# Optimization experiments

Hardware: AMD Instinct MI355X
Metric: run time of the kernel (lower is better)

Reference implementation:

```python
import jax, jax.numpy as jnp
import numpy as np

PI = np.float32(np.pi)
CNOT = jnp.array([[1,0,0,0],[0,1,0,0],[0,0,0,1],[0,0,1,0]], dtype=jnp.complex64)


def _u3(t, p, l):
    c, s = jnp.cos(t / 2), jnp.sin(t / 2)
    return jnp.stack([
        jnp.stack([c + 0j, -jnp.exp(1j * l) * s]),
        jnp.stack([jnp.exp(1j * p) * s, jnp.exp(1j * (p + l)) * c]),
    ]).astype(jnp.complex64)


def _ry(t):
    c, s = jnp.cos(t / 2), jnp.sin(t / 2)
    return jnp.stack([jnp.stack([c, -s]), jnp.stack([s, c])]).astype(jnp.complex64)


def _rz(t):
    z = jnp.zeros((), jnp.complex64)
    return jnp.stack([
        jnp.stack([jnp.exp(-1j * t / 2).astype(jnp.complex64), z]),
        jnp.stack([z, jnp.exp(1j * t / 2).astype(jnp.complex64)]),
    ]).astype(jnp.complex64)


def _apply1(psi, G, w):
    # psi: [N,2,2,2,2]; uniform single-qubit gate G [2,2] on wire w
    psi = jnp.moveaxis(psi, 1 + w, -1)
    psi = jnp.einsum('ij,nabcj->nabci', G, psi)
    return jnp.moveaxis(psi, -1, 1 + w)


def _apply1_batch(psi, G, w):
    # per-sample gate G [N,2,2]
    psi = jnp.moveaxis(psi, 1 + w, -1)
    psi = jnp.einsum('nij,nabcj->nabci', G, psi)
    return jnp.moveaxis(psi, -1, 1 + w)


def _apply2(psi, G, a, b):
    # two-qubit gate G [4,4] on wires (a,b)
    psi = jnp.moveaxis(psi, (1 + a, 1 + b), (-2, -1))
    psi = psi.reshape(psi.shape[:-2] + (4,))
    psi = jnp.einsum('ij,nabj->nabi', G, psi)
    psi = psi.reshape(psi.shape[:-1] + (2, 2))
    return jnp.moveaxis(psi, (-2, -1), (1 + a, 1 + b))


def _su4(psi, u3s, angs, a, b):
    # u3s: [4,3] = (w0, w1, w5, w6); angs: [3] = (w2, w3, w4)
    psi = _apply1(psi, _u3(u3s[0, 0], u3s[0, 1], u3s[0, 2]), a)
    psi = _apply1(psi, _u3(u3s[1, 0], u3s[1, 1], u3s[1, 2]), b)
    psi = _apply2(psi, CNOT, a, b)
    psi = _apply1(psi, _ry(angs[0]), a)
    psi = _apply1(psi, _rz(angs[1]), b)
    psi = _apply2(psi, CNOT, b, a)
    psi = _apply1(psi, _ry(angs[2]), a)
    psi = _apply2(psi, CNOT, a, b)
    psi = _apply1(psi, _u3(u3s[2, 0], u3s[2, 1], u3s[2, 2]), a)
    psi = _apply1(psi, _u3(u3s[3, 0], u3s[3, 1], u3s[3, 2]), b)
    return psi


def _circuit(angles, qw_u3, qw_ang):
    # angles: [N,4]; returns PauliZ expvals [N,4]
    N = angles.shape[0]
    psi = jnp.zeros((N, 2, 2, 2, 2), jnp.complex64).at[:, 0, 0, 0, 0].set(1.0)
    for w in range(4):  # AngleEmbedding: RY(angle) on each wire, per-sample
        c, s = jnp.cos(angles[:, w] / 2), jnp.sin(angles[:, w] / 2)
        G = jnp.stack([jnp.stack([c, -s], -1), jnp.stack([s, c], -1)], -2).astype(jnp.complex64)
        psi = _apply1_batch(psi, G, w)
    pairs = [(0, 1), (1, 2), (2, 3), (3, 0)]
    for layer in range(2):
        u3s = qw_u3[4 * layer:4 * layer + 4]
        angs = qw_ang[3 * layer:3 * layer + 3]
        for (a, b) in pairs:
            psi = _su4(psi, u3s, angs, a, b)
    p = psi.real ** 2 + psi.imag ** 2  # [N,2,2,2,2]
    z = jnp.array([1.0, -1.0], p.dtype)
    evs = [jnp.sum(p * z.reshape([1] + [2 if i == w else 1 for i in range(4)]), axis=(1, 2, 3, 4)) for w in range(4)]
    return jnp.stack(evs, -1)


def _conv(x, w, b):
    y = jax.lax.conv_general_dilated(x, w, (1, 1), 'SAME', dimension_numbers=('NCHW', 'OIHW', 'NCHW'))
    return y + b[None, :, None, None]


def _maxpool2(x):
    return jax.lax.reduce_window(x, -jnp.inf, jax.lax.max, (1, 1, 2, 2), (1, 1, 2, 2), 'VALID')


def setup_inputs() -> dict:
    key = jax.random.key(0)
    ks = jax.random.split(key, 20)
    n = jax.random.normal
    return {
        'x': n(ks[0], (1024, 3, 32, 32), jnp.float32),
        'conv1_w': n(ks[1], (64, 3, 3, 3), jnp.float32) * 0.1,
        'conv1_b': n(ks[2], (64,), jnp.float32) * 0.1,
        'conv2_w': n(ks[3], (16, 64, 3, 3), jnp.float32) * 0.05,
        'conv2_b': n(ks[4], (16,), jnp.float32) * 0.1,
        'conv3_w': n(ks[5], (4, 16, 3, 3), jnp.float32) * 0.1,
        'conv3_b': n(ks[6], (4,), jnp.float32) * 0.1,
        'qw_u3': jax.random.uniform(ks[7], (8, 3), jnp.float32, 0.0, 2 * np.pi),
        'qw_ang': jax.random.uniform(ks[8], (6,), jnp.float32, 0.0, 2 * np.pi),
        'fc1a_w': n(ks[9], (64, 256), jnp.float32) * 0.06,
        'fc1a_b': n(ks[10], (64,), jnp.float32) * 0.1,
        'fc1b_w': n(ks[11], (128, 64), jnp.float32) * 0.1,
        'fc1b_b': n(ks[12], (128,), jnp.float32) * 0.1,
        'fc2a_w': n(ks[13], (64, 128), jnp.float32) * 0.1,
        'fc2a_b': n(ks[14], (64,), jnp.float32) * 0.1,
        'fc2b_w': n(ks[15], (10, 64), jnp.float32) * 0.1,
        'fc2b_b': n(ks[16], (10,), jnp.float32) * 0.1,
    }


def reference(x, conv1_w, conv1_b, conv2_w, conv2_b, conv3_w, conv3_b,
              qw_u3, qw_ang, fc1a_w, fc1a_b, fc1b_w, fc1b_b,
              fc2a_w, fc2a_b, fc2b_w, fc2b_b):
    h = _maxpool2(jax.nn.relu(_conv(x, conv1_w, conv1_b)))      # [B,64,16,16]
    h = _maxpool2(jax.nn.relu(_conv(h, conv2_w, conv2_b)))      # [B,16,8,8]
    h = jax.nn.leaky_relu(_conv(h, conv3_w, conv3_b), 0.01)     # [B,4,8,8]
    B, C, H, W = h.shape
    # 1x1 patches in (h, w, c) order, matching torch unfold+permute
    patches = jnp.transpose(h, (0, 2, 3, 1)).reshape(B * H * W, C)
    ang = jax.nn.sigmoid(patches) * PI
    q = _circuit(ang, qw_u3, qw_ang)            # [B*64, 4]
    q = q.reshape(B, H * W * 4)                 # [B, 256]
    h1 = jax.nn.relu(q @ fc1a_w.T + fc1a_b)
    h1 = h1 @ fc1b_w.T + fc1b_b
    h2 = jax.nn.relu(h1 @ fc2a_w.T + fc2a_b)
    return h2 @ fc2b_w.T + fc2b_b               # [B, 10]
```

## Files before the change

kernel.cpp:

```cpp
#include <hip/hip_runtime.h>
#include <math.h>

#define PI_F 3.14159265358979323846f

typedef _Float16 half2_t __attribute__((ext_vector_type(2)));
typedef _Float16 f16x8 __attribute__((ext_vector_type(8)));
typedef float f32x4v __attribute__((ext_vector_type(4)));

__device__ __forceinline__ unsigned packh2(float lo, float hi) {
  unsigned short l = __builtin_bit_cast(unsigned short, (_Float16)lo);
  unsigned short h = __builtin_bit_cast(unsigned short, (_Float16)hi);
  return (unsigned)l | ((unsigned)h << 16);
}

struct c2 { float x, y; };
__device__ __forceinline__ c2 cmul(c2 a, c2 b){ return c2{a.x*b.x - a.y*b.y, a.x*b.y + a.y*b.x}; }
__device__ __forceinline__ c2 cadd(c2 a, c2 b){ return c2{a.x+b.x, a.y+b.y}; }

__device__ __forceinline__ void rot2(c2 &a, c2 &b, c2 g00, c2 g01, c2 g10, c2 g11) {
  c2 na = cadd(cmul(g00,a), cmul(g01,b));
  c2 nb = cadd(cmul(g10,a), cmul(g11,b));
  a = na; b = nb;
}

__device__ __forceinline__ void mk_u3(float th, float ph, float la,
                                      c2 &g00, c2 &g01, c2 &g10, c2 &g11) {
  float ch = cosf(0.5f*th), sh = sinf(0.5f*th);
  float cl = cosf(la), sl = sinf(la);
  float cp = cosf(ph), sp = sinf(ph);
  float cpl = cp*cl - sp*sl, spl = sp*cl + cp*sl;
  g00 = c2{ch, 0.f};
  g01 = c2{-cl*sh, -sl*sh};
  g10 = c2{cp*sh, sp*sh};
  g11 = c2{cpl*ch, spl*ch};
}

template<int MA, int MB>
__device__ __forceinline__ void apply2q(c2 psi[16], const c2 M[16]) {
#pragma unroll
  for (int r = 0; r < 16; ++r) {
    if (r & (MA | MB)) continue;
    c2 a = psi[r], b = psi[r|MB], c = psi[r|MA], d = psi[r|MA|MB];
    psi[r]        = cadd(cadd(cmul(M[0],a),  cmul(M[1],b)),  cadd(cmul(M[2],c),  cmul(M[3],d)));
    psi[r|MB]     = cadd(cadd(cmul(M[4],a),  cmul(M[5],b)),  cadd(cmul(M[6],c),  cmul(M[7],d)));
    psi[r|MA]     = cadd(cadd(cmul(M[8],a),  cmul(M[9],b)),  cadd(cmul(M[10],c), cmul(M[11],d)));
    psi[r|MA|MB]  = cadd(cadd(cmul(M[12],a), cmul(M[13],b)), cadd(cmul(M[14],c), cmul(M[15],d)));
  }
}

__global__ __launch_bounds__(256) void k_setup(const float* __restrict__ w1a, const float* __restrict__ w1b,
                                               const float* __restrict__ w2a, const float* __restrict__ w2b,
                                               const float* __restrict__ c2w,
                                               const float* __restrict__ c1w, const float* __restrict__ c1b,
                                               const float* __restrict__ qw_u3,
                                               const float* __restrict__ qw_ang,
                                               float* __restrict__ wt, float* __restrict__ A) {
  __shared__ c2 SU[2][16];
  __shared__ float Ur[16*17], Ui[16*17];
  int t = threadIdx.x;
  if (blockIdx.x == 167) {
    if (t < 8) {
      int L = t >> 2, col = t & 3;
      c2 s[4];
#pragma unroll
      for (int i = 0; i < 4; ++i) s[i] = c2{(i==col)?1.f:0.f, 0.f};
      const float* u = qw_u3 + 12*L;
      const float* g = qw_ang + 3*L;
      c2 g00,g01,g10,g11;
      mk_u3(u[0],u[1],u[2], g00,g01,g10,g11);
      rot2(s[0],s[2], g00,g01,g10,g11); rot2(s[1],s[3], g00,g01,g10,g11);
      mk_u3(u[3],u[4],u[5], g00,g01,g10,g11);
      rot2(s[0],s[1], g00,g01,g10,g11); rot2(s[2],s[3], g00,g01,g10,g11);
      { c2 tmp = s[2]; s[2] = s[3]; s[3] = tmp; }
      { float c = cosf(0.5f*g[0]), sn = sinf(0.5f*g[0]);
        c2 r00{c,0.f}, r01{-sn,0.f}, r10{sn,0.f}, r11{c,0.f};
        rot2(s[0],s[2], r00,r01,r10,r11); rot2(s[1],s[3], r00,r01,r10,r11); }
      { float c = cosf(0.5f*g[1]), sn = sinf(0.5f*g[1]);
        c2 e0{c,-sn}, e1{c,sn};
        s[0]=cmul(s[0],e0); s[1]=cmul(s[1],e1); s[2]=cmul(s[2],e0); s[3]=cmul(s[3],e1); }
      { c2 tmp = s[1]; s[1] = s[3]; s[3] = tmp; }
      { float c = cosf(0.5f*g[2]), sn = sinf(0.5f*g[2]);
        c2 r00{c,0.f}, r01{-sn,0.f}, r10{sn,0.f}, r11{c,0.f};
        rot2(s[0],s[2], r00,r01,r10,r11); rot2(s[1],s[3], r00,r01,r10,r11); }
      { c2 tmp = s[2]; s[2] = s[3]; s[3] = tmp; }
      mk_u3(u[6],u[7],u[8], g00,g01,g10,g11);
      rot2(s[0],s[2], g00,g01,g10,g11); rot2(s[1],s[3], g00,g01,g10,g11);
      mk_u3(u[9],u[10],u[11], g00,g01,g10,g11);
      rot2(s[0],s[1], g00,g01,g10,g11); rot2(s[2],s[3], g00,g01,g10,g11);
#pragma unroll
      for (int k = 0; k < 4; ++k) SU[L][k*4 + col] = s[k];
    }
    __syncthreads();
    if (t < 16) {
      c2 psi[16];
#pragma unroll
      for (int i = 0; i < 16; ++i) psi[i] = c2{(i==t)?1.f:0.f, 0.f};
#pragma unroll
      for (int l = 0; l < 2; ++l) {
        c2 M[16];
#pragma unroll
        for (int k = 0; k < 16; ++k) M[k] = SU[l][k];
        apply2q<8,4>(psi, M);
        apply2q<4,2>(psi, M);
        apply2q<2,1>(psi, M);
        apply2q<1,8>(psi, M);
      }
#pragma unroll
      for (int k = 0; k < 16; ++k) { Ur[k*17+t] = psi[k].x; Ui[k*17+t] = psi[k].y; }
    }
    __syncthreads();
    {
      int i = t >> 4, j = t & 15;
      float a0=0.f,a1=0.f,a2=0.f,a3=0.f;
#pragma unroll
      for (int k = 0; k < 16; ++k) {
        float pr = Ur[k*17+i]*Ur[k*17+j] + Ui[k*17+i]*Ui[k*17+j];
        a0 += ((k>>3)&1) ? -pr : pr;
        a1 += ((k>>2)&1) ? -pr : pr;
        a2 += ((k>>1)&1) ? -pr : pr;
        a3 += ( k     &1) ? -pr : pr;
      }
      A[0*256 + t] = a0; A[1*256 + t] = a1; A[2*256 + t] = a2; A[3*256 + t] = a3;
    }
    return;
  }
  int id = blockIdx.x*256 + t;
  if (id < 16384) { int j = id >> 6, o = id & 63;  wt[id] = w1a[o*256 + j]; return; }
  int id1 = id - 16384;
  if (id1 < 8192)  { int j = id1 >> 7, o = id1 & 127; wt[16384 + id1] = w1b[o*64 + j]; return; }
  int id2 = id1 - 8192;
  if (id2 < 8192)  { int j = id2 >> 6, o = id2 & 63;  wt[24576 + id2] = w2a[o*128 + j]; return; }
  int id3 = id2 - 8192;
  if (id3 < 640)   { int j = id3 / 10, o = id3 % 10;  wt[32768 + id3] = w2b[o*64 + j]; return; }
  int id4 = id3 - 640;
  if (id4 < 4608) {
    int s = id4 >> 8, rem = id4 & 255, l = rem >> 2, r = rem & 3;
    int tap = s >> 1, h = s & 1;
    int oc = l & 15, j = l >> 4;
    int icl = 16*h + 4*j + r;
    float lo = c2w[oc*576 + icl*9 + tap];
    float hi = c2w[oc*576 + (icl+32)*9 + tap];
    ((unsigned*)wt)[33408 + id4] = packh2(lo, hi);
    return;
  }
  int id5 = id4 - 4608;
  if (id5 < 1024) {
    int nt = id5 >> 8, rem = id5 & 255, l = rem >> 2, r = rem & 3;
    int oc = nt*16 + (l & 15), j = l >> 4;
    int k0 = 8*j + 2*r;
    float lo = (k0     < 27) ? c1w[oc*27 + k0]     : 0.f;
    float hi = (k0 + 1 < 27) ? c1w[oc*27 + k0 + 1] : 0.f;
    ((unsigned*)wt)[38016 + id5] = packh2(lo, hi);
  }
}

__global__ __launch_bounds__(512, 2) void k_conv12(
    const float* __restrict__ x,
    const uint4* __restrict__ B1g, const float* __restrict__ b1,
    const uint4* __restrict__ B2g, const float* __restrict__ b2,
    float* __restrict__ h2) {
  __shared__ float xs[3480];
  __shared__ unsigned hsp[11664];
  int b = blockIdx.x, t = threadIdx.x;
  int l = t & 63, w = t >> 6;
  int m = l & 15, j = l >> 4;
  uint4 Bf1[4];
#pragma unroll
  for (int nt = 0; nt < 4; ++nt) Bf1[nt] = B1g[nt*64 + l];
  float bz1[4];
#pragma unroll
  for (int nt = 0; nt < 4; ++nt) bz1[nt] = b1[nt*16 + m];
  int offs[8]; bool valid[8];
#pragma unroll
  for (int q = 0; q < 8; ++q) {
    int kk = 8*j + q;
    valid[q] = (kk < 27);
    int kc = valid[q] ? kk : 0;
    int c = kc / 9, rem = kc - 9*c, wr = rem / 3, cc = rem - 3*wr;
    offs[q] = c*1156 + wr*34 + cc;
  }
  for (int i = t; i < 3480; i += 512) xs[i] = 0.f;
  {
    uint4 z = make_uint4(0u,0u,0u,0u);
    uint4* hz = (uint4*)hsp;
    for (int i = t; i < 2916; i += 512) hz[i] = z;
  }
  __syncthreads();
  for (int i = t; i < 3072; i += 512) {
    int c = i >> 10, rem = i & 1023, gy = rem >> 5, gx = rem & 31;
    xs[c*1156 + (gy+1)*34 + gx + 1] = x[(size_t)b*3072 + i];
  }
  __syncthreads();
#pragma unroll
  for (int h = 0; h < 2; ++h) {
    f32x4v acc[2][2][4];
#pragma unroll
    for (int rr = 0; rr < 2; ++rr)
#pragma unroll
      for (int xh = 0; xh < 2; ++xh)
#pragma unroll
        for (int nt = 0; nt < 4; ++nt)
          acc[rr][xh][nt] = f32x4v{bz1[nt], bz1[nt], bz1[nt], bz1[nt]};
#pragma unroll
    for (int rr = 0; rr < 2; ++rr)
#pragma unroll
      for (int xh = 0; xh < 2; ++xh) {
        int base = (16*h + 2*w + rr)*34 + 16*xh + m;
        float v[8];
#pragma unroll
        for (int q = 0; q < 8; ++q) v[q] = valid[q] ? xs[offs[q] + base] : 0.f;
        unsigned a0 = packh2(v[0], v[1]), a1 = packh2(v[2], v[3]);
        unsigned a2u = packh2(v[4], v[5]), a3 = packh2(v[6], v[7]);
        uint4 Au = make_uint4(a0, a1, a2u, a3);
        f16x8 Av = __builtin_bit_cast(f16x8, Au);
#pragma unroll
        for (int nt = 0; nt < 4; ++nt)
          acc[rr][xh][nt] = __builtin_amdgcn_mfma_f32_16x16x32_f16(
              Av, __builtin_bit_cast(f16x8, Bf1[nt]), acc[rr][xh][nt], 0, 0, 0);
      }
    {
      int pyg = 8*h + w;
#pragma unroll
      for (int ntp = 0; ntp < 2; ++ntp)
#pragma unroll
        for (int xh = 0; xh < 2; ++xh)
#pragma unroll
          for (int pv = 0; pv < 2; ++pv) {
            f32x4v aL0 = acc[0][xh][ntp],   aL1 = acc[1][xh][ntp];
            f32x4v aH0 = acc[0][xh][ntp+2], aH1 = acc[1][xh][ntp+2];
            float mlo = fmaxf(fmaxf(aL0[2*pv], aL0[2*pv+1]), fmaxf(aL1[2*pv], aL1[2*pv+1]));
            float mhi = fmaxf(fmaxf(aH0[2*pv], aH0[2*pv+1]), fmaxf(aH1[2*pv], aH1[2*pv+1]));
            int px = 8*xh + 2*j + pv;
            hsp[((pyg+1)*18 + px + 1)*36 + ntp*16 + m] =
                packh2(fmaxf(mlo, 0.f), fmaxf(mhi, 0.f));
          }
    }
  }
  __syncthreads();
  uint4 Bf2[18];
#pragma unroll
  for (int s = 0; s < 18; ++s) Bf2[s] = B2g[s*64 + l];
  float bz2 = b2[m];
  f32x4v a2[2];
  a2[0] = f32x4v{bz2, bz2, bz2, bz2};
  a2[1] = f32x4v{bz2, bz2, bz2, bz2};
#pragma unroll
  for (int s = 0; s < 18; ++s) {
    const int tap = s >> 1, hh = s & 1;
    const int dy = tap / 3, dx = tap % 3;
    f16x8 Bv = __builtin_bit_cast(f16x8, Bf2[s]);
#pragma unroll
    for (int tt = 0; tt < 2; ++tt) {
      int y = 2*w + tt;
      f16x8 Av = __builtin_bit_cast(f16x8,
          *(const uint4*)(hsp + ((y+dy)*18 + m + dx)*36 + 16*hh + 4*j));
      a2[tt] = __builtin_amdgcn_mfma_f32_16x16x32_f16(Av, Bv, a2[tt], 0, 0, 0);
    }
  }
  float* outb = h2 + (size_t)b*1024 + m*64;
#pragma unroll
  for (int vp = 0; vp < 2; ++vp) {
    float mm = fmaxf(fmaxf(a2[0][2*vp], a2[0][2*vp+1]),
                     fmaxf(a2[1][2*vp], a2[1][2*vp+1]));
    outb[w*8 + 2*j + vp] = fmaxf(mm, 0.f);
  }
}

__global__ __launch_bounds__(256) void k_tail(const float* __restrict__ h2, const float* __restrict__ w,
                                              const float* __restrict__ bias, const float* __restrict__ Ag,
                                              const float* __restrict__ wt,
                                              const float* __restrict__ b1a, const float* __restrict__ b1b,
                                              const float* __restrict__ b2a, const float* __restrict__ b2b,
                                              float* __restrict__ out) {
  __shared__ float h3s[1600];
  __shared__ float As[1024];
  __shared__ float c3s[4][64];
  __shared__ float qs[256];
  __shared__ float red[256];
  __shared__ float h1s[64];
  __shared__ float hbv[128];
  __shared__ float h3v[64];
  int b = blockIdx.x, t = threadIdx.x;
#pragma unroll
  for (int k = 0; k < 4; ++k) As[t + ((k + (t>>6)) & 3)*256 - 0] = As[t + ((k + (t>>6)) & 3)*256 - 0];
#pragma unroll
  for (int k = 0; k < 4; ++k) As[k*256 + t] = Ag[k*256 + t];
  for (int i = t; i < 1600; i += 256) h3s[i] = 0.f;
  __syncthreads();
  {
    const float4* src = (const float4*)(h2 + (size_t)b*1024);
    float4 v = src[t];
    int e = 4*t;
    int ic = e >> 6, iy = (e >> 3) & 7, ix = e & 7;
    float* d = &h3s[ic*100 + (iy+1)*10 + ix + 1];
    d[0]=v.x; d[1]=v.y; d[2]=v.z; d[3]=v.w;
  }
  __syncthreads();
  {
    int oc = t >> 6, pos = t & 63;
    int y = pos >> 3, xo = pos & 7;
    float acc = bias[oc];
    const float* wp = w + oc*144;
    for (int ic = 0; ic < 16; ++ic) {
#pragma unroll
      for (int ky = 0; ky < 3; ++ky)
#pragma unroll
        for (int kx = 0; kx < 3; ++kx)
          acc = fmaf(wp[ic*9 + ky*3 + kx], h3s[ic*100 + (y+ky)*10 + (xo+kx)], acc);
    }
    c3s[oc][pos] = acc;
  }
  __syncthreads();
  {
    int p = t & 63, w4 = t >> 6;
    float v0[2], v1[2], v2[2], v3[2];
#pragma unroll
    for (int o = 0; o < 4; ++o) {
      float v = c3s[o][p];
      float lv = v > 0.f ? v : 0.01f*v;
      float sg = 1.f/(1.f + expf(-lv));
      float sv, cv;
      __sincosf(sg * (0.5f*PI_F), &sv, &cv);
      float* dst = (o==0)?v0:(o==1)?v1:(o==2)?v2:v3;
      dst[0] = cv; dst[1] = sv;
    }
    float pv[16];
#pragma unroll
    for (int i = 0; i < 16; ++i)
      pv[i] = v0[(i>>3)&1] * v1[(i>>2)&1] * v2[(i>>1)&1] * v3[i&1];
    const float4* Aw = (const float4*)(As + w4*256);
    float a = 0.f;
#pragma unroll
    for (int i = 0; i < 16; ++i) {
      float d = 0.f;
#pragma unroll
      for (int j4 = 0; j4 < 4; ++j4) {
        float4 av = Aw[i*4 + j4];
        d = fmaf(av.x, pv[j4*4+0], d);
        d = fmaf(av.y, pv[j4*4+1], d);
        d = fmaf(av.z, pv[j4*4+2], d);
        d = fmaf(av.w, pv[j4*4+3], d);
      }
      a = fmaf(pv[i], d, a);
    }
    qs[p*4 + w4] = a;
  }
  __syncthreads();
  const float* WT1a = wt;
  const float* WT1b = wt + 16384;
  const float* WT2a = wt + 24576;
  const float* WT2b = wt + 32768;
  {
    int o = t & 63, seg = t >> 6;
    float acc = 0.f;
    const float* wp = WT1a + seg*64*64 + o;
    const float* qp = qs + seg*64;
    for (int jj = 0; jj < 64; ++jj) acc = fmaf(wp[jj*64], qp[jj], acc);
    red[seg*64 + o] = acc;
  }
  __syncthreads();
  if (t < 64) {
    float s = red[t] + red[64+t] + red[128+t] + red[192+t] + b1a[t];
    h1s[t] = fmaxf(s, 0.f);
  }
  __syncthreads();
  if (t < 128) {
    float acc = b1b[t];
    for (int j = 0; j < 64; ++j) acc = fmaf(WT1b[j*128 + t], h1s[j], acc);
    hbv[t] = acc;
  }
  __syncthreads();
  {
    int o = t & 63, seg = t >> 6;
    float acc = 0.f;
    const float* wp = WT2a + seg*32*64 + o;
    const float* hp = hbv + seg*32;
    for (int jj = 0; jj < 32; ++jj) acc = fmaf(wp[jj*64], hp[jj], acc);
    red[seg*64 + o] = acc;
  }
  __syncthreads();
  if (t < 64) {
    float s = red[t] + red[64+t] + red[128+t] + red[192+t] + b2a[t];
    h3v[t] = fmaxf(s, 0.f);
  }
  __syncthreads();
  if (t < 10) {
    float o = b2b[t];
    for (int j = 0; j < 64; ++j) o = fmaf(WT2b[j*10 + t], h3v[j], o);
    out[(size_t)b*10 + t] = o;
  }
}

extern "C" void kernel_launch(void* const* d_in, const int* in_sizes, int n_in,
                              void* d_out, int out_size, void* d_ws, size_t ws_size,
                              hipStream_t stream) {
  const float* x       = (const float*)d_in[0];
  const float* conv1_w = (const float*)d_in[1];
  const float* conv1_b = (const float*)d_in[2];
  const float* conv2_w = (const float*)d_in[3];
  const float* conv2_b = (const float*)d_in[4];
  const float* conv3_w = (const float*)d_in[5];
  const float* conv3_b = (const float*)d_in[6];
  const float* qw_u3   = (const float*)d_in[7];
  const float* qw_ang  = (const float*)d_in[8];
  const float* fc1a_w  = (const float*)d_in[9];
  const float* fc1a_b  = (const float*)d_in[10];
  const float* fc1b_w  = (const float*)d_in[11];
  const float* fc1b_b  = (const float*)d_in[12];
  const float* fc2a_w  = (const float*)d_in[13];
  const float* fc2a_b  = (const float*)d_in[14];
  const float* fc2b_w  = (const float*)d_in[15];
  const float* fc2b_b  = (const float*)d_in[16];
  float* out = (float*)d_out;

  float* ws  = (float*)d_ws;
  float* A   = ws;
  float* WT  = ws + 1024;
  const uint4* BG  = (const uint4*)((const unsigned*)WT + 33408);
  const uint4* B1G = (const uint4*)((const unsigned*)WT + 38016);
  float* h2  = ws + 17083008;

  k_setup <<<168,  256, 0, stream>>>(fc1a_w, fc1b_w, fc2a_w, fc2b_w, conv2_w, conv1_w, conv1_b,
                                     qw_u3, qw_ang, WT, A);
  k_conv12<<<1024, 512, 0, stream>>>(x, B1G, conv1_b, BG, conv2_b, h2);
  k_tail  <<<1024, 256, 0, stream>>>(h2, conv3_w, conv3_b, A, WT,
                                     fc1a_b, fc1b_b, fc2a_b, fc2b_b, out);
}
```

Measured before the change: 48.22 us.

## Fuse conv1/conv2 kernel with conv3, quantum circuit and FC tail

Merges the conv12 and tail kernels into one kernel per sample. The conv2 output stays in shared memory, with the xs and hsp buffers reused for the tail's working arrays, instead of going through a global h2 buffer. This removes one kernel launch and a global write and read of the intermediate. The cost is that the tail phases run on a 512-thread block where only up to 256 threads do work, and the extra barriers may lengthen the per-block critical path.

```diff
diff --git a/kernel.cpp b/kernel.cpp
--- a/kernel.cpp
+++ b/kernel.cpp
@@ -154,13 +154,26 @@
   }
 }
 
-__global__ __launch_bounds__(512, 2) void k_conv12(
+__global__ __launch_bounds__(512, 2) void k_fused(
     const float* __restrict__ x,
     const uint4* __restrict__ B1g, const float* __restrict__ b1,
     const uint4* __restrict__ B2g, const float* __restrict__ b2,
-    float* __restrict__ h2) {
+    const float* __restrict__ w3, const float* __restrict__ b3,
+    const float* __restrict__ Ag, const float* __restrict__ wt,
+    const float* __restrict__ b1a, const float* __restrict__ b1b,
+    const float* __restrict__ b2a, const float* __restrict__ b2b,
+    float* __restrict__ out) {
   __shared__ float xs[3480];
   __shared__ unsigned hsp[11664];
+  float* h2l = xs;
+  float* h3s = (float*)hsp;
+  float* As  = (float*)hsp + 1600;
+  float* c3s = (float*)hsp + 2624;
+  float* qs  = (float*)hsp + 2880;
+  float* red = (float*)hsp + 3136;
+  float* h1s = (float*)hsp + 3392;
+  float* hbv = (float*)hsp + 3456;
+  float* h3v = (float*)hsp + 3584;
   int b = blockIdx.x, t = threadIdx.x;
   int l = t & 63, w = t >> 6;
   int m = l & 15, j = l >> 4;
@@ -209,9 +222,8 @@
         float v[8];
 #pragma unroll
         for (int q = 0; q < 8; ++q) v[q] = valid[q] ? xs[offs[q] + base] : 0.f;
-        unsigned a0 = packh2(v[0], v[1]), a1 = packh2(v[2], v[3]);
-        unsigned a2u = packh2(v[4], v[5]), a3 = packh2(v[6], v[7]);
-        uint4 Au = make_uint4(a0, a1, a2u, a3);
+        uint4 Au = make_uint4(packh2(v[0], v[1]), packh2(v[2], v[3]),
+                              packh2(v[4], v[5]), packh2(v[6], v[7]));
         f16x8 Av = __builtin_bit_cast(f16x8, Au);
 #pragma unroll
         for (int nt = 0; nt < 4; ++nt)
@@ -237,70 +249,54 @@
     }
   }
   __syncthreads();
-  uint4 Bf2[18];
-#pragma unroll
-  for (int s = 0; s < 18; ++s) Bf2[s] = B2g[s*64 + l];
-  float bz2 = b2[m];
-  f32x4v a2[2];
-  a2[0] = f32x4v{bz2, bz2, bz2, bz2};
-  a2[1] = f32x4v{bz2, bz2, bz2, bz2};
-#pragma unroll
-  for (int s = 0; s < 18; ++s) {
-    const int tap = s >> 1, hh = s & 1;
-    const int dy = tap / 3, dx = tap % 3;
-    f16x8 Bv = __builtin_bit_cast(f16x8, Bf2[s]);
-#pragma unroll
-    for (int tt = 0; tt < 2; ++tt) {
-      int y = 2*w + tt;
-      f16x8 Av = __builtin_bit_cast(f16x8,
-          *(const uint4*)(hsp + ((y+dy)*18 + m + dx)*36 + 16*hh + 4*j));
-      a2[tt] = __builtin_amdgcn_mfma_f32_16x16x32_f16(Av, Bv, a2[tt], 0, 0, 0);
-    }
-  }
-  float* outb = h2 + (size_t)b*1024 + m*64;
-#pragma unroll
-  for (int vp = 0; vp < 2; ++vp) {
-    float mm = fmaxf(fmaxf(a2[0][2*vp], a2[0][2*vp+1]),
-                     fmaxf(a2[1][2*vp], a2[1][2*vp+1]));
-    outb[w*8 + 2*j + vp] = fmaxf(mm, 0.f);
-  }
-}
-
-__global__ __launch_bounds__(256) void k_tail(const float* __restrict__ h2, const float* __restrict__ w,
-                                              const float* __restrict__ bias, const float* __restrict__ Ag,
-                                              const float* __restrict__ wt,
-                                              const float* __restrict__ b1a, const float* __restrict__ b1b,
-                                              const float* __restrict__ b2a, const float* __restrict__ b2b,
-                                              float* __restrict__ out) {
-  __shared__ float h3s[1600];
-  __shared__ float As[1024];
-  __shared__ float c3s[4][64];
-  __shared__ float qs[256];
-  __shared__ float red[256];
-  __shared__ float h1s[64];
-  __shared__ float hbv[128];
-  __shared__ float h3v[64];
-  int b = blockIdx.x, t = threadIdx.x;
-#pragma unroll
-  for (int k = 0; k < 4; ++k) As[t + ((k + (t>>6)) & 3)*256 - 0] = As[t + ((k + (t>>6)) & 3)*256 - 0];
-#pragma unroll
-  for (int k = 0; k < 4; ++k) As[k*256 + t] = Ag[k*256 + t];
-  for (int i = t; i < 1600; i += 256) h3s[i] = 0.f;
-  __syncthreads();
   {
-    const float4* src = (const float4*)(h2 + (size_t)b*1024);
-    float4 v = src[t];
-    int e = 4*t;
-    int ic = e >> 6, iy = (e >> 3) & 7, ix = e & 7;
-    float* d = &h3s[ic*100 + (iy+1)*10 + ix + 1];
-    d[0]=v.x; d[1]=v.y; d[2]=v.z; d[3]=v.w;
-  }
-  __syncthreads();
-  {
+    uint4 Bf2[18];
+#pragma unroll
+    for (int s = 0; s < 18; ++s) Bf2[s] = B2g[s*64 + l];
+    float bz2 = b2[m];
+    f32x4v a2[2];
+    a2[0] = f32x4v{bz2, bz2, bz2, bz2};
+    a2[1] = f32x4v{bz2, bz2, bz2, bz2};
+#pragma unroll
+    for (int s = 0; s < 18; ++s) {
+      const int tap = s >> 1, hh = s & 1;
+      const int dy = tap / 3, dx = tap % 3;
+      f16x8 Bv = __builtin_bit_cast(f16x8, Bf2[s]);
+#pragma unroll
+      for (int tt = 0; tt < 2; ++tt) {
+        int y = 2*w + tt;
+        f16x8 Av = __builtin_bit_cast(f16x8,
+            *(const uint4*)(hsp + ((y+dy)*18 + m + dx)*36 + 16*hh + 4*j));
+        a2[tt] = __builtin_amdgcn_mfma_f32_16x16x32_f16(Av, Bv, a2[tt], 0, 0, 0);
+      }
+    }
+    __syncthreads();
+#pragma unroll
+    for (int vp = 0; vp < 2; ++vp) {
+      float mm = fmaxf(fmaxf(a2[0][2*vp], a2[0][2*vp+1]),
+                       fmaxf(a2[1][2*vp], a2[1][2*vp+1]));
+      h2l[(w*8 + 2*j + vp)*16 + m] = fmaxf(mm, 0.f);
+    }
+  }
+  __syncthreads();
+  for (int i = t; i < 1600; i += 512) h3s[i] = 0.f;
+  for (int i = t; i < 1024; i += 512) As[i] = Ag[i];
+  __syncthreads();
+  if (t < 256) {
+    int pos = t >> 2, ic0 = 4*(t & 3);
+    int iy = pos >> 3, ix = pos & 7;
+    float4 v = *(const float4*)&h2l[pos*16 + ic0];
+    h3s[(ic0+0)*100 + (iy+1)*10 + ix + 1] = v.x;
+    h3s[(ic0+1)*100 + (iy+1)*10 + ix + 1] = v.y;
+    h3s[(ic0+2)*100 + (iy+1)*10 + ix + 1] = v.z;
+    h3s[(ic0+3)*100 + (iy+1)*10 + ix + 1] = v.w;
+  }
+  __syncthreads();
+  if (t < 256) {
     int oc = t >> 6, pos = t & 63;
     int y = pos >> 3, xo = pos & 7;
-    float acc = bias[oc];
-    const float* wp = w + oc*144;
+    float acc = b3[oc];
+    const float* wp = w3 + oc*144;
     for (int ic = 0; ic < 16; ++ic) {
 #pragma unroll
       for (int ky = 0; ky < 3; ++ky)
@@ -308,15 +304,15 @@
         for (int kx = 0; kx < 3; ++kx)
           acc = fmaf(wp[ic*9 + ky*3 + kx], h3s[ic*100 + (y+ky)*10 + (xo+kx)], acc);
     }
-    c3s[oc][pos] = acc;
-  }
-  __syncthreads();
-  {
+    c3s[oc*64 + pos] = acc;
+  }
+  __syncthreads();
+  if (t < 256) {
     int p = t & 63, w4 = t >> 6;
     float v0[2], v1[2], v2[2], v3[2];
 #pragma unroll
     for (int o = 0; o < 4; ++o) {
-      float v = c3s[o][p];
+      float v = c3s[o*64 + p];
       float lv = v > 0.f ? v : 0.01f*v;
       float sg = 1.f/(1.f + expf(-lv));
       float sv, cv;
@@ -350,7 +346,7 @@
   const float* WT1b = wt + 16384;
   const float* WT2a = wt + 24576;
   const float* WT2b = wt + 32768;
-  {
+  if (t < 256) {
     int o = t & 63, seg = t >> 6;
     float acc = 0.f;
     const float* wp = WT1a + seg*64*64 + o;
@@ -366,11 +362,11 @@
   __syncthreads();
   if (t < 128) {
     float acc = b1b[t];
-    for (int j = 0; j < 64; ++j) acc = fmaf(WT1b[j*128 + t], h1s[j], acc);
+    for (int jj = 0; jj < 64; ++jj) acc = fmaf(WT1b[jj*128 + t], h1s[jj], acc);
     hbv[t] = acc;
   }
   __syncthreads();
-  {
+  if (t < 256) {
     int o = t & 63, seg = t >> 6;
     float acc = 0.f;
     const float* wp = WT2a + seg*32*64 + o;
@@ -386,7 +382,7 @@
   __syncthreads();
   if (t < 10) {
     float o = b2b[t];
-    for (int j = 0; j < 64; ++j) o = fmaf(WT2b[j*10 + t], h3v[j], o);
+    for (int jj = 0; jj < 64; ++jj) o = fmaf(WT2b[jj*10 + t], h3v[jj], o);
     out[(size_t)b*10 + t] = o;
   }
 }
@@ -418,11 +414,10 @@
   float* WT  = ws + 1024;
   const uint4* BG  = (const uint4*)((const unsigned*)WT + 33408);
   const uint4* B1G = (const uint4*)((const unsigned*)WT + 38016);
-  float* h2  = ws + 17083008;
-
-  k_setup <<<168,  256, 0, stream>>>(fc1a_w, fc1b_w, fc2a_w, fc2b_w, conv2_w, conv1_w, conv1_b,
-                                     qw_u3, qw_ang, WT, A);
-  k_conv12<<<1024, 512, 0, stream>>>(x, B1G, conv1_b, BG, conv2_b, h2);
-  k_tail  <<<1024, 256, 0, stream>>>(h2, conv3_w, conv3_b, A, WT,
-                                     fc1a_b, fc1b_b, fc2a_b, fc2b_b, out);
-}
+
+  k_setup<<<168,  256, 0, stream>>>(fc1a_w, fc1b_w, fc2a_w, fc2b_w, conv2_w, conv1_w, conv1_b,
+                                    qw_u3, qw_ang, WT, A);
+  k_fused<<<1024, 512, 0, stream>>>(x, B1G, conv1_b, BG, conv2_b,
+                                    conv3_w, conv3_b, A, WT,
+                                    fc1a_b, fc1b_b, fc2a_b, fc2b_b, out);
+}
```

New measurement: 67.47 us. +39.9%, slower.
